# Performance work log

Measured on AMD Instinct MI355X. Metric: run time of the kernel, lower is better.

The kernel has to match this reference:

```python
import jax, jax.numpy as jnp
import numpy as np

S, L, B = 64, 64, 16
D_IN, D_ATTN = 1024, 512


def setup_inputs() -> dict:
    key = jax.random.key(0)
    ks = jax.random.split(key, 8)
    context = jax.random.normal(ks[0], (S, L, B, D_IN), dtype=jnp.float32)
    query = jax.random.normal(ks[1], (L, B, D_IN), dtype=jnp.float32)
    mask = jnp.ones((S, L, B), dtype=jnp.int32)
    # Linear params (torch layout: weight [out, in], bias [out])
    sc = 1.0 / np.sqrt(D_IN)
    Wc = jax.random.uniform(ks[2], (D_ATTN, D_IN), minval=-sc, maxval=sc, dtype=jnp.float32)
    bc = jax.random.uniform(ks[3], (D_ATTN,), minval=-sc, maxval=sc, dtype=jnp.float32)
    Wq = jax.random.uniform(ks[4], (D_ATTN, D_IN), minval=-sc, maxval=sc, dtype=jnp.float32)
    bq = jax.random.uniform(ks[5], (D_ATTN,), minval=-sc, maxval=sc, dtype=jnp.float32)
    v = jax.random.uniform(ks[6], (D_ATTN,), dtype=jnp.float32)  # torch.rand -> U[0,1)
    return {"context": context, "query": query, "mask": mask,
            "Wc": Wc, "bc": bc, "Wq": Wq, "bq": bq, "v": v}


def reference(context, query, mask, Wc, bc, Wq, bq, v):
    # context: [s,l,b,din], query: [l,b,din]
    context_proj = jnp.einsum('slbi,di->slbd', context, Wc) + bc  # [s,l,b,da]
    query_proj = jnp.einsum('lbi,di->lbd', query, Wq) + bq        # [l,b,da]
    scores = jnp.tanh(context_proj + query_proj[None])            # [s,l,b,da]
    scores = jnp.einsum('slbd,d->slb', scores, v)                 # [s,l,b]
    scores = jnp.where(mask == 0, jnp.float32(-1e9), scores)
    alpha = jax.nn.softmax(scores, axis=0)                        # softmax over s
    attn_output = jnp.einsum('slb,slbd->lbd', alpha, context)     # [l,b,din]
    return (attn_output, alpha)
```

## Files before the change

kernel.cpp:

```cpp
#include <hip/hip_runtime.h>
#include <hip/hip_fp16.h>
#include <stdint.h>

#define S_DIM 64
#define L_DIM 64
#define B_DIM 16
#define LB    1024
#define DIN   1024
#define DA    512
#define M_TOT 65536

using f16x8 = __attribute__((ext_vector_type(8))) _Float16;
using f32x4 = __attribute__((ext_vector_type(4))) float;

typedef const __attribute__((address_space(1))) void* gas_ptr;
typedef __attribute__((address_space(3))) void* las_ptr;

__device__ __forceinline__ void load_lds16(const void* g, void* l) {
    __builtin_amdgcn_global_load_lds((gas_ptr)g, (las_ptr)l, 16, 0, 0);
}

__device__ __forceinline__ float fast_tanh(float x) {
    return 1.0f - 2.0f / (__expf(2.0f * x) + 1.0f);
}

__global__ void cvt_all(const float* __restrict__ Wc, const float* __restrict__ Wq,
                        const float* __restrict__ q,
                        _Float16* __restrict__ Wch, _Float16* __restrict__ Wqh,
                        _Float16* __restrict__ Qh) {
    int i = blockIdx.x * 256 + threadIdx.x;
    if (i < DA * DIN)            Wch[i] = (_Float16)Wc[i];
    else if (i < 2 * DA * DIN)   Wqh[i - DA * DIN] = (_Float16)Wq[i - DA * DIN];
    else                         Qh[i - 2 * DA * DIN] = (_Float16)q[i - 2 * DA * DIN];
}

__global__ __launch_bounds__(256) void qp_gemm(
    const _Float16* __restrict__ Qh,
    const _Float16* __restrict__ Wqh,
    const float* __restrict__ bq, const float* __restrict__ bc,
    float* __restrict__ qp)
{
    __shared__ __align__(16) _Float16 lA[64 * 64];
    __shared__ __align__(16) _Float16 lB[64 * 64];
    const int t = threadIdx.x;
    const int w = t >> 6, lane = t & 63;
    const int quad = lane >> 4, m16 = lane & 15;
    const int n0 = blockIdx.x * 64, lb0 = blockIdx.y * 64;

    f32x4 acc[4] = {};

    for (int kt = 0; kt < DIN / 64; ++kt) {
#pragma unroll
        for (int i = 0; i < 2; ++i) {
            int c = (w * 2 + i) * 64 + lane;
            int row = c >> 3;
            int kc = (c & 7) ^ (row & 7);
            load_lds16(Qh  + (size_t)(lb0 + row) * DIN + kt * 64 + kc * 8, (char*)lA + (size_t)c * 16);
            load_lds16(Wqh + (size_t)(n0  + row) * DIN + kt * 64 + kc * 8, (char*)lB + (size_t)c * 16);
        }
        __syncthreads();
#pragma unroll
        for (int kk = 0; kk < 64; kk += 32) {
            int cq = (kk >> 3) + quad;
            int ar = 16 * w + m16;
            f16x8 a = *(const f16x8*)((const char*)lA + ar * 128 + ((cq ^ (ar & 7)) * 16));
#pragma unroll
            for (int j = 0; j < 4; ++j) {
                int br = 16 * j + m16;
                f16x8 b = *(const f16x8*)((const char*)lB + br * 128 + ((cq ^ (br & 7)) * 16));
                acc[j] = __builtin_amdgcn_mfma_f32_16x16x32_f16(a, b, acc[j], 0, 0, 0);
            }
        }
        __syncthreads();
    }
#pragma unroll
    for (int j = 0; j < 4; ++j) {
        int n = n0 + 16 * j + m16;
        float bias = bq[n] + bc[n];
#pragma unroll
        for (int r = 0; r < 4; ++r) {
            int lb = lb0 + 16 * w + quad * 4 + r;
            qp[(size_t)lb * DA + n] = acc[j][r] + bias;
        }
    }
}

__global__ __launch_bounds__(256) void score_gemm3(
    const float* __restrict__ ctx,
    const _Float16* __restrict__ Wch,
    const float* __restrict__ qp,
    const float* __restrict__ v,
    float* __restrict__ sc4)
{
    __shared__ __align__(16) _Float16 lA[128 * 64];
    __shared__ __align__(16) _Float16 lB[128 * 64];
    __shared__ float lP[2][128];

    const int t = threadIdx.x;
    const int w = t >> 6, lane = t & 63;
    const int quad = lane >> 4, m16 = lane & 15;
    const int wm = w & 1, wn = w >> 1;

    int bid = blockIdx.x;
    int xcd = bid & 7;
    int j2 = bid >> 3;
    int nq = j2 & 3;
    int mb = ((j2 >> 2) << 3) | xcd;
    const int m0 = mb * 128;
    const int n0 = nq * 128;

    f32x4 acc[4][4] = {};

    const int arow = t >> 1;
    const int acol = t & 1;
    const float* gA = ctx + (size_t)(m0 + arow) * DIN + acol * 32;

    f32x4 fA[8];
#pragma unroll
    for (int qd = 0; qd < 8; ++qd) fA[qd] = *(const f32x4*)(gA + qd * 4);

#pragma unroll 1
    for (int kt = 0; kt < DIN / 64; ++kt) {
        if (kt) __syncthreads();
#pragma unroll
        for (int i = 0; i < 4; ++i) {
            int c = (w * 4 + i) * 64 + lane;
            int row = c >> 3;
            int kc = (c & 7) ^ (row & 7);
            load_lds16(Wch + (size_t)(n0 + row) * DIN + kt * 64 + kc * 8,
                       (char*)lB + (size_t)c * 16);
        }
#pragma unroll
        for (int q2 = 0; q2 < 4; ++q2) {
            f16x8 h = {(_Float16)fA[2*q2][0], (_Float16)fA[2*q2][1],
                       (_Float16)fA[2*q2][2], (_Float16)fA[2*q2][3],
                       (_Float16)fA[2*q2+1][0], (_Float16)fA[2*q2+1][1],
                       (_Float16)fA[2*q2+1][2], (_Float16)fA[2*q2+1][3]};
            int c = acol * 4 + q2;
            *(f16x8*)((char*)lA + arow * 128 + ((c ^ (arow & 7)) * 16)) = h;
        }
        __syncthreads();
        if (kt < DIN / 64 - 1) {
            const float* p = gA + (kt + 1) * 64;
#pragma unroll
            for (int qd = 0; qd < 8; ++qd) fA[qd] = *(const f32x4*)(p + qd * 4);
        }
#pragma unroll
        for (int kk = 0; kk < 64; kk += 32) {
            int cq = (kk >> 3) + quad;
            f16x8 a[4], b[4];
#pragma unroll
            for (int i = 0; i < 4; ++i) {
                int ar = wm * 64 + 16 * i + m16;
                a[i] = *(const f16x8*)((const char*)lA + ar * 128 + ((cq ^ (ar & 7)) * 16));
            }
#pragma unroll
            for (int j = 0; j < 4; ++j) {
                int br = wn * 64 + 16 * j + m16;
                b[j] = *(const f16x8*)((const char*)lB + br * 128 + ((cq ^ (br & 7)) * 16));
            }
#pragma unroll
            for (int i = 0; i < 4; ++i)
#pragma unroll
                for (int j = 0; j < 4; ++j)
                    acc[i][j] = __builtin_amdgcn_mfma_f32_16x16x32_f16(a[i], b[j], acc[i][j], 0, 0, 0);
        }
    }

    float vv[4];
    int nn[4];
#pragma unroll
    for (int j = 0; j < 4; ++j) { nn[j] = n0 + wn * 64 + 16 * j + m16; vv[j] = v[nn[j]]; }

    float part[16];
#pragma unroll
    for (int i = 0; i < 4; ++i) {
#pragma unroll
        for (int r = 0; r < 4; ++r) {
            int gm = m0 + wm * 64 + 16 * i + quad * 4 + r;
            int lb = gm & (LB - 1);
            float s = 0.f;
#pragma unroll
            for (int j = 0; j < 4; ++j) {
                float x = acc[i][j][r] + qp[(size_t)lb * DA + nn[j]];
                s += fast_tanh(x) * vv[j];
            }
            part[i * 4 + r] = s;
        }
    }
#pragma unroll
    for (int off = 1; off < 16; off <<= 1) {
#pragma unroll
        for (int k = 0; k < 16; ++k) part[k] += __shfl_xor(part[k], off, 64);
    }
    if (m16 == 0) {
#pragma unroll
        for (int k = 0; k < 16; ++k) {
            int row_local = wm * 64 + 16 * (k >> 2) + quad * 4 + (k & 3);
            lP[wn][row_local] = part[k];
        }
    }
    __syncthreads();
    if (t < 128) {
        float s = lP[0][t] + lP[1][t];
        sc4[(size_t)nq * M_TOT + m0 + t] = s;
    }
}

__global__ __launch_bounds__(256) void softmax_ws(
    const float* __restrict__ sc4, const int* __restrict__ mask,
    const float* __restrict__ ctx,
    float* __restrict__ alpha_out, float* __restrict__ attn_out) {
    __shared__ float lAl[S_DIM];
    const int lb = blockIdx.x;
    const int t = threadIdx.x;
    if (t < S_DIM) {
        int s = t;
        int idx = s * LB + lb;
        float x = sc4[idx] + sc4[M_TOT + idx] + sc4[2 * M_TOT + idx] + sc4[3 * M_TOT + idx];
        if (mask[idx] == 0) x = -1e9f;
        float mx = x;
#pragma unroll
        for (int off = 1; off < 64; off <<= 1) mx = fmaxf(mx, __shfl_xor(mx, off, 64));
        float e = __expf(x - mx);
        float sum = e;
#pragma unroll
        for (int off = 1; off < 64; off <<= 1) sum += __shfl_xor(sum, off, 64);
        float a = e / sum;
        alpha_out[idx] = a;
        lAl[s] = a;
    }
    __syncthreads();
    f32x4 acc = {0.f, 0.f, 0.f, 0.f};
    const float* base = ctx + (size_t)lb * DIN + t * 4;
#pragma unroll 4
    for (int s = 0; s < S_DIM; ++s) {
        float a = lAl[s];
        f32x4 c = *(const f32x4*)(base + (size_t)s * LB * DIN);
        acc += a * c;
    }
    *(f32x4*)(attn_out + (size_t)lb * DIN + t * 4) = acc;
}

extern "C" void kernel_launch(void* const* d_in, const int* in_sizes, int n_in,
                              void* d_out, int out_size, void* d_ws, size_t ws_size,
                              hipStream_t stream) {
    (void)in_sizes; (void)n_in; (void)out_size; (void)ws_size;
    const float* ctx   = (const float*)d_in[0];
    const float* query = (const float*)d_in[1];
    const int*   mask  = (const int*)d_in[2];
    const float* Wc    = (const float*)d_in[3];
    const float* bc    = (const float*)d_in[4];
    const float* Wq    = (const float*)d_in[5];
    const float* bq    = (const float*)d_in[6];
    const float* v     = (const float*)d_in[7];

    float* out_attn  = (float*)d_out;
    float* out_alpha = (float*)d_out + (size_t)LB * DIN;

    char* ws = (char*)d_ws;
    _Float16* Wch = (_Float16*)(ws);
    _Float16* Wqh = (_Float16*)(ws + (1 << 20));
    _Float16* Qh  = (_Float16*)(ws + (2 << 20));
    float*    qp  = (float*)(ws + (4 << 20));
    float*    sc4 = (float*)(ws + (6 << 20));

    cvt_all<<<(2 * DA * DIN + LB * DIN) / 256, 256, 0, stream>>>(Wc, Wq, query, Wch, Wqh, Qh);
    qp_gemm<<<dim3(DA / 64, LB / 64), 256, 0, stream>>>(Qh, Wqh, bq, bc, qp);
    score_gemm3<<<2048, 256, 0, stream>>>(ctx, Wch, qp, v, sc4);
    softmax_ws<<<LB, 256, 0, stream>>>(sc4, mask, ctx, out_alpha, out_attn);
}
```

Baseline: 549.2 us.

## Compute full N per block to read context once, double-buffer weight tiles

Each block now covers all 512 attention columns for 128 context rows instead of one quarter, so the fp32 context is streamed from memory once rather than four times, and the cross-quarter score buffer is removed. Weight tiles for the full N width are double-buffered in LDS and prefetched one K-step ahead. The cost is a 256-element accumulator per thread, about 144KB of LDS, occupancy of one block per CU, and fewer blocks to hide latency.

```diff
diff --git a/kernel.cpp b/kernel.cpp
--- a/kernel.cpp
+++ b/kernel.cpp
@@ -85,36 +85,35 @@
     }
 }
 
-__global__ __launch_bounds__(256) void score_gemm3(
+__global__ __launch_bounds__(256, 1) void score_gemm4(
     const float* __restrict__ ctx,
     const _Float16* __restrict__ Wch,
     const float* __restrict__ qp,
     const float* __restrict__ v,
-    float* __restrict__ sc4)
+    float* __restrict__ sc)
 {
     __shared__ __align__(16) _Float16 lA[128 * 64];
-    __shared__ __align__(16) _Float16 lB[128 * 64];
-    __shared__ float lP[2][128];
+    __shared__ __align__(16) _Float16 lB[2][512 * 64];
+    __shared__ float lP[4][128];
 
     const int t = threadIdx.x;
     const int w = t >> 6, lane = t & 63;
     const int quad = lane >> 4, m16 = lane & 15;
-    const int wm = w & 1, wn = w >> 1;
-
-    int bid = blockIdx.x;
-    int xcd = bid & 7;
-    int j2 = bid >> 3;
-    int nq = j2 & 3;
-    int mb = ((j2 >> 2) << 3) | xcd;
-    const int m0 = mb * 128;
-    const int n0 = nq * 128;
-
-    f32x4 acc[4][4] = {};
+    const int m0 = blockIdx.x * 128;
+
+    f32x4 acc[8][8] = {};
 
     const int arow = t >> 1;
     const int acol = t & 1;
     const float* gA = ctx + (size_t)(m0 + arow) * DIN + acol * 32;
 
+#pragma unroll
+    for (int i = 0; i < 16; ++i) {
+        int c = (w * 16 + i) * 64 + lane;
+        int row = c >> 3;
+        int kc = (c & 7) ^ (row & 7);
+        load_lds16(Wch + (size_t)row * DIN + kc * 8, (char*)lB[0] + (size_t)c * 16);
+    }
     f32x4 fA[8];
 #pragma unroll
     for (int qd = 0; qd < 8; ++qd) fA[qd] = *(const f32x4*)(gA + qd * 4);
@@ -122,14 +121,6 @@
 #pragma unroll 1
     for (int kt = 0; kt < DIN / 64; ++kt) {
         if (kt) __syncthreads();
-#pragma unroll
-        for (int i = 0; i < 4; ++i) {
-            int c = (w * 4 + i) * 64 + lane;
-            int row = c >> 3;
-            int kc = (c & 7) ^ (row & 7);
-            load_lds16(Wch + (size_t)(n0 + row) * DIN + kt * 64 + kc * 8,
-                       (char*)lB + (size_t)c * 16);
-        }
 #pragma unroll
         for (int q2 = 0; q2 < 4; ++q2) {
             f16x8 h = {(_Float16)fA[2*q2][0], (_Float16)fA[2*q2][1],
@@ -141,48 +132,59 @@
         }
         __syncthreads();
         if (kt < DIN / 64 - 1) {
+            const _Float16* gB = Wch + (kt + 1) * 64;
+            char* dB = (char*)lB[(kt + 1) & 1];
+#pragma unroll
+            for (int i = 0; i < 16; ++i) {
+                int c = (w * 16 + i) * 64 + lane;
+                int row = c >> 3;
+                int kc = (c & 7) ^ (row & 7);
+                load_lds16(gB + (size_t)row * DIN + kc * 8, dB + (size_t)c * 16);
+            }
             const float* p = gA + (kt + 1) * 64;
 #pragma unroll
             for (int qd = 0; qd < 8; ++qd) fA[qd] = *(const f32x4*)(p + qd * 4);
         }
+        const char* bbuf = (const char*)lB[kt & 1];
 #pragma unroll
         for (int kk = 0; kk < 64; kk += 32) {
             int cq = (kk >> 3) + quad;
-            f16x8 a[4], b[4];
-#pragma unroll
-            for (int i = 0; i < 4; ++i) {
-                int ar = wm * 64 + 16 * i + m16;
+            f16x8 a[8], b[8];
+#pragma unroll
+            for (int i = 0; i < 8; ++i) {
+                int ar = 16 * i + m16;
                 a[i] = *(const f16x8*)((const char*)lA + ar * 128 + ((cq ^ (ar & 7)) * 16));
             }
 #pragma unroll
-            for (int j = 0; j < 4; ++j) {
-                int br = wn * 64 + 16 * j + m16;
-                b[j] = *(const f16x8*)((const char*)lB + br * 128 + ((cq ^ (br & 7)) * 16));
-            }
-#pragma unroll
-            for (int i = 0; i < 4; ++i)
-#pragma unroll
-                for (int j = 0; j < 4; ++j)
+            for (int j = 0; j < 8; ++j) {
+                int br = w * 128 + 16 * j + m16;
+                b[j] = *(const f16x8*)(bbuf + br * 128 + ((cq ^ (br & 7)) * 16));
+            }
+#pragma unroll
+            for (int i = 0; i < 8; ++i)
+#pragma unroll
+                for (int j = 0; j < 8; ++j)
                     acc[i][j] = __builtin_amdgcn_mfma_f32_16x16x32_f16(a[i], b[j], acc[i][j], 0, 0, 0);
         }
     }
 
-    float vv[4];
-    int nn[4];
-#pragma unroll
-    for (int j = 0; j < 4; ++j) { nn[j] = n0 + wn * 64 + 16 * j + m16; vv[j] = v[nn[j]]; }
-
-    float part[16];
-#pragma unroll
-    for (int i = 0; i < 4; ++i) {
+    float vv[8];
+    int nn[8];
+#pragma unroll
+    for (int j = 0; j < 8; ++j) { nn[j] = w * 128 + 16 * j + m16; vv[j] = v[nn[j]]; }
+
+    float part[32];
+#pragma unroll
+    for (int i = 0; i < 8; ++i) {
 #pragma unroll
         for (int r = 0; r < 4; ++r) {
-            int gm = m0 + wm * 64 + 16 * i + quad * 4 + r;
+            int gm = m0 + 16 * i + quad * 4 + r;
             int lb = gm & (LB - 1);
+            const float* qrow = qp + (size_t)lb * DA;
             float s = 0.f;
 #pragma unroll
-            for (int j = 0; j < 4; ++j) {
-                float x = acc[i][j][r] + qp[(size_t)lb * DA + nn[j]];
+            for (int j = 0; j < 8; ++j) {
+                float x = acc[i][j][r] + qrow[nn[j]];
                 s += fast_tanh(x) * vv[j];
             }
             part[i * 4 + r] = s;
@@ -191,24 +193,23 @@
 #pragma unroll
     for (int off = 1; off < 16; off <<= 1) {
 #pragma unroll
-        for (int k = 0; k < 16; ++k) part[k] += __shfl_xor(part[k], off, 64);
+        for (int k = 0; k < 32; ++k) part[k] += __shfl_xor(part[k], off, 64);
     }
     if (m16 == 0) {
 #pragma unroll
-        for (int k = 0; k < 16; ++k) {
-            int row_local = wm * 64 + 16 * (k >> 2) + quad * 4 + (k & 3);
-            lP[wn][row_local] = part[k];
+        for (int k = 0; k < 32; ++k) {
+            int row_local = 16 * (k >> 2) + quad * 4 + (k & 3);
+            lP[w][row_local] = part[k];
         }
     }
     __syncthreads();
     if (t < 128) {
-        float s = lP[0][t] + lP[1][t];
-        sc4[(size_t)nq * M_TOT + m0 + t] = s;
+        sc[m0 + t] = lP[0][t] + lP[1][t] + lP[2][t] + lP[3][t];
     }
 }
 
 __global__ __launch_bounds__(256) void softmax_ws(
-    const float* __restrict__ sc4, const int* __restrict__ mask,
+    const float* __restrict__ sc, const int* __restrict__ mask,
     const float* __restrict__ ctx,
     float* __restrict__ alpha_out, float* __restrict__ attn_out) {
     __shared__ float lAl[S_DIM];
@@ -217,7 +218,7 @@
     if (t < S_DIM) {
         int s = t;
         int idx = s * LB + lb;
-        float x = sc4[idx] + sc4[M_TOT + idx] + sc4[2 * M_TOT + idx] + sc4[3 * M_TOT + idx];
+        float x = sc[idx];
         if (mask[idx] == 0) x = -1e9f;
         float mx = x;
 #pragma unroll
@@ -263,10 +264,10 @@
     _Float16* Wqh = (_Float16*)(ws + (1 << 20));
     _Float16* Qh  = (_Float16*)(ws + (2 << 20));
     float*    qp  = (float*)(ws + (4 << 20));
-    float*    sc4 = (float*)(ws + (6 << 20));
+    float*    sc  = (float*)(ws + (6 << 20));
 
     cvt_all<<<(2 * DA * DIN + LB * DIN) / 256, 256, 0, stream>>>(Wc, Wq, query, Wch, Wqh, Qh);
     qp_gemm<<<dim3(DA / 64, LB / 64), 256, 0, stream>>>(Qh, Wqh, bq, bc, qp);
-    score_gemm3<<<2048, 256, 0, stream>>>(ctx, Wch, qp, v, sc4);
-    softmax_ws<<<LB, 256, 0, stream>>>(sc4, mask, ctx, out_alpha, out_attn);
-}
+    score_gemm4<<<M_TOT / 128, 256, 0, stream>>>(ctx, Wch, qp, v, sc);
+    softmax_ws<<<LB, 256, 0, stream>>>(sc, mask, ctx, out_alpha, out_attn);
+}
```

New measurement: 699.2 us. 27.3% more time.
